# Kernel optimization log

Hardware: AMD Instinct MI355X
Metric: run time of the kernel (lower is better)

The kernel has to match this reference:

```python
import jax, jax.numpy as jnp
import numpy as np

EMBED = 512
NHEAD = 16
HDIM = EMBED // NHEAD
HIDDEN = 512  # Mlp hidden is hard-coded to 512
EPS_LN = 1e-6
EPS_ATT = 1e-6


def layernorm(x, gamma, beta):
    mu = jnp.mean(x, axis=-1, keepdims=True)
    var = jnp.mean(jnp.square(x - mu), axis=-1, keepdims=True)
    return (x - mu) * jax.lax.rsqrt(var + EPS_LN) * gamma + beta


def setup_inputs() -> dict:
    key = jax.random.key(0)
    ks = jax.random.split(key, 16)
    B, N, C = 8, 4096, EMBED
    s = 1.0 / np.sqrt(C)
    inp = {
        "x": jax.random.normal(ks[0], (B, N, C), dtype=jnp.float32),
        # projection weights stored as (in, out); torch Linear uses x @ W.T
        "Wq": jax.random.normal(ks[1], (C, C), dtype=jnp.float32) * s,
        "Wk": jax.random.normal(ks[2], (C, C), dtype=jnp.float32) * s,
        "Wv": jax.random.normal(ks[3], (C, C), dtype=jnp.float32) * s,
        "Wm": jax.random.normal(ks[4], (C, C), dtype=jnp.float32) * s,
        "W1": jax.random.normal(ks[5], (C, HIDDEN), dtype=jnp.float32) * s,
        "b1": jax.random.normal(ks[6], (HIDDEN,), dtype=jnp.float32) * 1e-6,
        "W2": jax.random.normal(ks[7], (HIDDEN, C), dtype=jnp.float32) * (1.0 / np.sqrt(HIDDEN)),
        "b2": jax.random.normal(ks[8], (C,), dtype=jnp.float32) * 1e-6,
        "g_att": jnp.ones((C,), dtype=jnp.float32),
        "b_att": jnp.zeros((C,), dtype=jnp.float32),
        "g_ffn": jnp.ones((C,), dtype=jnp.float32),
        "b_ffn": jnp.zeros((C,), dtype=jnp.float32),
    }
    return inp


def reference(x, Wq, Wk, Wv, Wm, W1, b1, W2, b2, g_att, b_att, g_ffn, b_ffn):
    B, N, C = x.shape
    # --- attention sub-block ---
    h = layernorm(x, g_att, b_att)
    q = (h @ Wq).reshape(B, N, NHEAD, HDIM)
    k = (h @ Wk).reshape(B, N, NHEAD, HDIM)
    v = (h @ Wv).reshape(B, N, NHEAD, HDIM)
    Q = jax.nn.elu(q) + 1.0  # feature map: elu(x)+1
    K = jax.nn.elu(k) + 1.0
    v = v / N
    KV = jnp.einsum('nshd,nshv->nhdv', K, v)
    Z = 1.0 / (jnp.einsum('nlhd,nhd->nlh', Q, K.sum(axis=1)) + EPS_ATT)
    msg = jnp.einsum('nlhd,nhdv->nlhv', Q, KV) * Z[..., None] * N
    msg = msg.reshape(B, N, C) @ Wm
    x = x + msg
    # --- feed-forward sub-block ---
    h2 = layernorm(x, g_ffn, b_ffn)
    f = jax.nn.gelu(h2 @ W1 + b1, approximate=False) @ W2 + b2
    return x + f
```

## Files before the change

### kernel.cpp

```cpp
#include <hip/hip_runtime.h>
#include <hip/hip_bf16.h>
#include <math.h>

typedef unsigned short u16;
typedef __attribute__((ext_vector_type(8))) __bf16 bf16x8;
typedef __attribute__((ext_vector_type(4))) float floatx4;

#define SEQ   4096
#define BATCH 8
#define ROWS  32768
#define C     512
#define NH    16
#define HD    32

__device__ inline u16 f2bf(float f) {
    union { float f; unsigned u; } v; v.f = f;
    unsigned r = (v.u + 0x7FFFu + ((v.u >> 16) & 1u)) >> 16;
    return (u16)r;
}
__device__ inline float bf2f(u16 h) {
    union { unsigned u; float f; } v; v.u = ((unsigned)h) << 16;
    return v.f;
}

__device__ inline void g2lds16(const u16* g, u16* l) {
    __builtin_amdgcn_global_load_lds((const __attribute__((address_space(1))) unsigned*)g,
                                     (__attribute__((address_space(3))) unsigned*)l, 16, 0, 0);
}

__global__ __launch_bounds__(256) void prep_weights(
    const float* __restrict__ Wq, const float* __restrict__ Wk,
    const float* __restrict__ Wv, const float* __restrict__ Wm,
    const float* __restrict__ W1, const float* __restrict__ W2,
    u16* __restrict__ Wqkvt, u16* __restrict__ Wmt,
    u16* __restrict__ W1t, u16* __restrict__ W2t)
{
    int blk = blockIdx.x;
    int mat = blk >> 6;
    int tile = blk & 63;
    int k0 = (tile >> 3) * 64, n0 = (tile & 7) * 64;
    const float* src; u16* dst;
    switch (mat) {
        case 0: src = Wq; dst = Wqkvt;              break;
        case 1: src = Wk; dst = Wqkvt + 512*512;    break;
        case 2: src = Wv; dst = Wqkvt + 2*512*512;  break;
        case 3: src = Wm; dst = Wmt;                break;
        case 4: src = W1; dst = W1t;                break;
        default: src = W2; dst = W2t;               break;
    }
    __shared__ float ts[64][65];
    int t = threadIdx.x;
    #pragma unroll
    for (int i = 0; i < 16; i++) {
        int e = i * 256 + t;
        int kr = e >> 6, nc = e & 63;
        ts[kr][nc] = src[(size_t)(k0 + kr) * 512 + n0 + nc];
    }
    __syncthreads();
    #pragma unroll
    for (int i = 0; i < 2; i++) {
        int e = i * 256 + t;
        int nr = e >> 3, kc0 = (e & 7) * 8;
        union { uint4 v; u16 u[8]; } o;
        #pragma unroll
        for (int q = 0; q < 8; q++) o.u[q] = f2bf(ts[kc0 + q][nr]);
        *(uint4*)(dst + (size_t)(n0 + nr) * 512 + k0 + kc0) = o.v;
    }
}

__global__ __launch_bounds__(256) void ln_kernel(
    const float* __restrict__ in, const float* __restrict__ g,
    const float* __restrict__ b, u16* __restrict__ out)
{
    int row  = blockIdx.x * 4 + (threadIdx.x >> 6);
    int lane = threadIdx.x & 63;
    const float* p = in + (size_t)row * C + lane * 8;
    float4 v0 = *(const float4*)p;
    float4 v1 = *(const float4*)(p + 4);
    float s  = v0.x + v0.y + v0.z + v0.w + v1.x + v1.y + v1.z + v1.w;
    float s2 = v0.x*v0.x + v0.y*v0.y + v0.z*v0.z + v0.w*v0.w
             + v1.x*v1.x + v1.y*v1.y + v1.z*v1.z + v1.w*v1.w;
    #pragma unroll
    for (int off = 1; off < 64; off <<= 1) {
        s  += __shfl_xor(s, off);
        s2 += __shfl_xor(s2, off);
    }
    float mean = s * (1.f / C);
    float var  = s2 * (1.f / C) - mean * mean;
    float inv  = rsqrtf(var + 1e-6f);
    int c = lane * 8;
    float4 g0 = *(const float4*)(g + c), g1 = *(const float4*)(g + c + 4);
    float4 b0 = *(const float4*)(b + c), b1 = *(const float4*)(b + c + 4);
    union { uint4 v; u16 u[8]; } o;
    o.u[0] = f2bf((v0.x - mean) * inv * g0.x + b0.x);
    o.u[1] = f2bf((v0.y - mean) * inv * g0.y + b0.y);
    o.u[2] = f2bf((v0.z - mean) * inv * g0.z + b0.z);
    o.u[3] = f2bf((v0.w - mean) * inv * g0.w + b0.w);
    o.u[4] = f2bf((v1.x - mean) * inv * g1.x + b1.x);
    o.u[5] = f2bf((v1.y - mean) * inv * g1.y + b1.y);
    o.u[6] = f2bf((v1.z - mean) * inv * g1.z + b1.z);
    o.u[7] = f2bf((v1.w - mean) * inv * g1.w + b1.w);
    *(uint4*)(out + (size_t)row * C + c) = o.v;
}

template <int EPI>
__global__ __launch_bounds__(256, 2) void gemm_tile(
    const u16* __restrict__ A, const u16* __restrict__ Bt,
    int K, int ldc, int nyt,
    u16* __restrict__ outb, float* __restrict__ outf,
    const float* __restrict__ bias, const float* __restrict__ resid)
{
    __shared__ u16 lsA[128 * 64];
    __shared__ u16 lsB[128 * 64];
    const int t = threadIdx.x;
    const int w = t >> 6, l = t & 63, lr = l & 15, quad = l >> 4;
    const int g = blockIdx.x;
    const int xcd = g & 7;
    const int q = g >> 3;
    const int per = nyt >> 3;
    const int ty = xcd * per + (q % per);
    const int tx = q / per;
    const int m0 = ty * 128, n0 = tx * 128;
    const int RW = (w >> 1) * 64, CW = (w & 1) * 64;

    floatx4 acc[4][4];
    #pragma unroll
    for (int i = 0; i < 4; i++)
        #pragma unroll
        for (int j = 0; j < 4; j++) { floatx4 z = {0.f, 0.f, 0.f, 0.f}; acc[i][j] = z; }

    const int srow = w * 32 + (l >> 3);
    const int scol = (((l & 7) - (l >> 3)) & 7) * 8;
    const u16* Ag = A  + (size_t)(m0 + srow) * K + scol;
    const u16* Bg = Bt + (size_t)(n0 + srow) * K + scol;
    u16* lAw = lsA + w * 2048;
    u16* lBw = lsB + w * 2048;

    for (int kk = 0; kk < K; kk += 64) {
        __syncthreads();
        #pragma unroll
        for (int c = 0; c < 4; c++) {
            g2lds16(Ag + (size_t)(c * 8) * K + kk, lAw + c * 512);
            g2lds16(Bg + (size_t)(c * 8) * K + kk, lBw + c * 512);
        }
        __syncthreads();
        #pragma unroll
        for (int ks = 0; ks < 2; ks++) {
            bf16x8 af[4], bfr[4];
            const int m = ((ks * 4 + quad + (lr & 7)) & 7) * 8;
            #pragma unroll
            for (int i = 0; i < 4; i++) {
                af[i]  = *(const bf16x8*)(lsA + (RW + i * 16 + lr) * 64 + m);
                bfr[i] = *(const bf16x8*)(lsB + (CW + i * 16 + lr) * 64 + m);
            }
            #pragma unroll
            for (int i = 0; i < 4; i++)
                #pragma unroll
                for (int j = 0; j < 4; j++)
                    acc[i][j] = __builtin_amdgcn_mfma_f32_16x16x32_bf16(af[i], bfr[j], acc[i][j], 0, 0, 0);
        }
    }

    #pragma unroll
    for (int i = 0; i < 4; i++) {
        #pragma unroll
        for (int j = 0; j < 4; j++) {
            #pragma unroll
            for (int r = 0; r < 4; r++) {
                int row = m0 + RW + i * 16 + quad * 4 + r;
                int col = n0 + CW + j * 16 + lr;
                float v = acc[i][j][r];
                size_t idx = (size_t)row * ldc + col;
                if constexpr (EPI == 0) {
                    if (col < 1024) v = v > 0.f ? v + 1.f : __expf(v);
                    else            v *= (1.0f / SEQ);
                    outb[idx] = f2bf(v);
                } else if constexpr (EPI == 1) {
                    outf[idx] = resid[idx] + v;
                } else if constexpr (EPI == 2) {
                    v += bias[col];
                    v = 0.5f * v * (1.f + erff(v * 0.70710678118f));
                    outb[idx] = f2bf(v);
                } else {
                    outf[idx] = outf[idx] + v + bias[col];
                }
            }
        }
    }
}

__global__ __launch_bounds__(256) void kv_reduce(
    const u16* __restrict__ qkv, float* __restrict__ Pkv, float* __restrict__ PKsum)
{
    const int bh = blockIdx.x;
    const int b = bh >> 4, h = bh & 15;
    const int chunk = blockIdx.y;
    const int t = threadIdx.x;
    const int w = t >> 6, l = t & 63, lr = l & 15, quad = l >> 4;
    __shared__ u16 lds[4 * 2 * 2048];

    const int sbase = chunk * 512 + w * 128;
    const u16* qbase = qkv + (size_t)b * SEQ * 1536 + 512 + h * HD;

    const int sl0 = l >> 2;
    const int sl1 = 16 + sl0;
    const int cl  = l & 3;
    const int cg0 = (cl + (sl0 >> 3)) & 3;
    const int cg1 = (cl + (sl1 >> 3)) & 3;
    const int gof0 = sl0 * 1536 + cg0 * 8;
    const int gof1 = sl1 * 1536 + cg1 * 8;

    u16* myl = lds + w * 4096;

    const int offA0 = quad * 256 + ((((lr >> 3) + 0) - quad) & 3) * 8 + (lr & 7);
    const int offA1 = quad * 256 + ((((lr >> 3) + 2) - quad) & 3) * 8 + (lr & 7);

    floatx4 a00 = {0,0,0,0}, a01 = {0,0,0,0}, a10 = {0,0,0,0}, a11 = {0,0,0,0};
    float ks0 = 0.f, ks1 = 0.f;

    {
        const u16* gK = qbase + (size_t)sbase * 1536;
        g2lds16(gK + gof0,       myl);
        g2lds16(gK + gof1,       myl + 512);
        g2lds16(gK + 512 + gof0, myl + 1024);
        g2lds16(gK + 512 + gof1, myl + 1536);
    }
    #pragma unroll
    for (int st = 0; st < 4; st++) {
        if (st < 3) {
            const u16* gK = qbase + (size_t)(sbase + (st + 1) * 32) * 1536;
            u16* nl = myl + ((st + 1) & 1) * 2048;
            g2lds16(gK + gof0,       nl);
            g2lds16(gK + gof1,       nl + 512);
            g2lds16(gK + 512 + gof0, nl + 1024);
            g2lds16(gK + 512 + gof1, nl + 1536);
        }
        __syncthreads();
        const u16* lK = myl + (st & 1) * 2048;
        const u16* lV = lK + 1024;
        union { bf16x8 v; u16 u[8]; } fa0, fa1, fb0, fb1;
        #pragma unroll
        for (int j = 0; j < 8; j++) {
            fa0.u[j] = lK[offA0 + j * 32];
            fa1.u[j] = lK[offA1 + j * 32];
            fb0.u[j] = lV[offA0 + j * 32];
            fb1.u[j] = lV[offA1 + j * 32];
        }
        #pragma unroll
        for (int j = 0; j < 8; j++) { ks0 += bf2f(fa0.u[j]); ks1 += bf2f(fa1.u[j]); }
        a00 = __builtin_amdgcn_mfma_f32_16x16x32_bf16(fa0.v, fb0.v, a00, 0, 0, 0);
        a01 = __builtin_amdgcn_mfma_f32_16x16x32_bf16(fa0.v, fb1.v, a01, 0, 0, 0);
        a10 = __builtin_amdgcn_mfma_f32_16x16x32_bf16(fa1.v, fb0.v, a10, 0, 0, 0);
        a11 = __builtin_amdgcn_mfma_f32_16x16x32_bf16(fa1.v, fb1.v, a11, 0, 0, 0);
    }

    const int p = bh * 32 + chunk * 4 + w;
    float* dst = Pkv + (size_t)p * 1024;
    floatx4 accs[2][2] = {{a00, a01}, {a10, a11}};
    #pragma unroll
    for (int i = 0; i < 2; i++)
        #pragma unroll
        for (int j = 0; j < 2; j++)
            #pragma unroll
            for (int r = 0; r < 4; r++)
                dst[(i * 16 + quad * 4 + r) * 32 + j * 16 + lr] = accs[i][j][r];

    float k0 = ks0 + __shfl_xor(ks0, 16); k0 += __shfl_xor(k0, 32);
    float k1 = ks1 + __shfl_xor(ks1, 16); k1 += __shfl_xor(k1, 32);
    if (quad == 0) {
        PKsum[p * 32 + lr]      = k0;
        PKsum[p * 32 + 16 + lr] = k1;
    }
}

__global__ __launch_bounds__(256) void kv_final(
    const float* __restrict__ Pkv, const float* __restrict__ PKsum,
    float* __restrict__ KV, float* __restrict__ Ksum)
{
    const int bh = blockIdx.x;
    const int t = threadIdx.x;
    float a0 = 0.f, a1 = 0.f, a2 = 0.f, a3 = 0.f;
    for (int p = 0; p < 32; p++) {
        const float* src = Pkv + ((size_t)bh * 32 + p) * 1024;
        a0 += src[t];
        a1 += src[t + 256];
        a2 += src[t + 512];
        a3 += src[t + 768];
    }
    float* dst = KV + (size_t)bh * 1024;
    dst[t] = a0; dst[t + 256] = a1; dst[t + 512] = a2; dst[t + 768] = a3;
    if (t < 32) {
        float s = 0.f;
        for (int p = 0; p < 32; p++) s += PKsum[(bh * 32 + p) * 32 + t];
        Ksum[bh * 32 + t] = s;
    }
}

__global__ __launch_bounds__(256) void msg_kernel(
    const u16* __restrict__ qkv, const float* __restrict__ KV,
    const float* __restrict__ Ksum, u16* __restrict__ msg)
{
    int blk = blockIdx.x;
    int b = blk >> 7;
    int r0 = (blk & 127) * 32;
    int t = threadIdx.x;
    int h = t >> 4;
    int vd = (t & 15) * 2;
    float kv0[32], kv1[32], ksr[32];
    const float* kvh = KV + ((size_t)b * 16 + h) * 1024;
    const float* ksh = Ksum + (b * 16 + h) * 32;
    #pragma unroll
    for (int d = 0; d < 32; d++) {
        kv0[d] = kvh[d * 32 + vd];
        kv1[d] = kvh[d * 32 + vd + 1];
        ksr[d] = ksh[d];
    }
    __shared__ u16 Qs[4 * 512];
    const int srr = t >> 6;
    const int scc = (t & 63) * 8;
    for (int rg = 0; rg < 32; rg += 4) {
        size_t row = (size_t)b * SEQ + r0 + rg;
        uint4 qv = *(const uint4*)(qkv + (row + srr) * 1536 + scc);
        __syncthreads();
        *(uint4*)(Qs + srr * 512 + scc) = qv;
        __syncthreads();
        #pragma unroll
        for (int r2 = 0; r2 < 4; r2++) {
            const u16* qp = Qs + r2 * 512 + h * HD;
            float q[32];
            #pragma unroll
            for (int i0 = 0; i0 < 32; i0 += 8) {
                union { uint4 v; u16 u[8]; } uu;
                uu.v = *(const uint4*)(qp + i0);
                #pragma unroll
                for (int jq = 0; jq < 8; jq++) q[i0 + jq] = bf2f(uu.u[jq]);
            }
            float zdot = 0.f, m0 = 0.f, m1 = 0.f;
            #pragma unroll
            for (int d = 0; d < 32; d++) {
                float qd = q[d];
                zdot += qd * ksr[d];
                m0   += qd * kv0[d];
                m1   += qd * kv1[d];
            }
            float z = (float)SEQ / (zdot + 1e-6f);
            unsigned pack = (unsigned)f2bf(m0 * z) | ((unsigned)f2bf(m1 * z) << 16);
            *(unsigned*)(msg + (row + r2) * C + h * HD + vd) = pack;
        }
    }
}

extern "C" void kernel_launch(void* const* d_in, const int* in_sizes, int n_in,
                              void* d_out, int out_size, void* d_ws, size_t ws_size,
                              hipStream_t stream) {
    const float* x     = (const float*)d_in[0];
    const float* Wq    = (const float*)d_in[1];
    const float* Wk    = (const float*)d_in[2];
    const float* Wv    = (const float*)d_in[3];
    const float* Wm    = (const float*)d_in[4];
    const float* W1    = (const float*)d_in[5];
    const float* b1    = (const float*)d_in[6];
    const float* W2    = (const float*)d_in[7];
    const float* b2    = (const float*)d_in[8];
    const float* g_att = (const float*)d_in[9];
    const float* b_att = (const float*)d_in[10];
    const float* g_ffn = (const float*)d_in[11];
    const float* b_ffn = (const float*)d_in[12];
    float* out = (float*)d_out;

    char* ws = (char*)d_ws;
    u16*   Wqkvt = (u16*)(ws);
    u16*   Wmt   = (u16*)(ws + 0x180000);
    u16*   W1t   = (u16*)(ws + 0x200000);
    u16*   W2t   = (u16*)(ws + 0x280000);
    float* KV    = (float*)(ws + 0x300000);
    float* Ksum  = (float*)(ws + 0x380000);
    u16*   hb    = (u16*)(ws + 0x400000);
    float* Pkv   = (float*)(ws + 0x400000);
    float* PKsum = (float*)(ws + 0x1400000);
    u16*   qkv   = (u16*)(ws + 0x2400000);
    u16*   h2    = qkv;
    u16*   f1    = (u16*)(ws + 0x4400000);

    prep_weights<<<6 * 64, 256, 0, stream>>>(Wq, Wk, Wv, Wm, W1, W2,
                                             Wqkvt, Wmt, W1t, W2t);
    ln_kernel<<<ROWS / 4, 256, 0, stream>>>(x, g_att, b_att, hb);
    gemm_tile<0><<<12 * 256, 256, 0, stream>>>(hb, Wqkvt, 512, 1536, 256,
                                               qkv, nullptr, nullptr, nullptr);
    kv_reduce<<<dim3(128, 8), 256, 0, stream>>>(qkv, Pkv, PKsum);
    kv_final<<<128, 256, 0, stream>>>(Pkv, PKsum, KV, Ksum);
    msg_kernel<<<1024, 256, 0, stream>>>(qkv, KV, Ksum, hb);
    gemm_tile<1><<<4 * 256, 256, 0, stream>>>(hb, Wmt, 512, 512, 256,
                                              nullptr, out, nullptr, x);
    ln_kernel<<<ROWS / 4, 256, 0, stream>>>(out, g_ffn, b_ffn, h2);
    gemm_tile<2><<<4 * 256, 256, 0, stream>>>(h2, W1t, 512, 512, 256,
                                              f1, nullptr, b1, nullptr);
    gemm_tile<3><<<4 * 256, 256, 0, stream>>>(f1, W2t, 512, 512, 256,
                                              nullptr, out, b2, nullptr);
}
```

Before: 405.2 us.

## Replace 128x128 GEMM with 256x256 double-buffered, phase-pipelined 8-wave kernel

Replaces the single-buffered 128x128 GEMM tile with a 256x256 tile computed by 512 threads. The LDS is double-buffered and the work is split into quadrant phases, so global-to-LDS loads for later k-steps overlap the MFMA work, using explicit waitcnt, barriers and setprio. The larger tile raises operand reuse and cuts the number of blocks, but it uses more LDS and registers and hard-codes K=512 and the grid mapping. With 256 blocks for the N=512 GEMMs there may be barely one wave of blocks across the CUs.

```diff
diff --git a/kernel.cpp b/kernel.cpp
--- a/kernel.cpp
+++ b/kernel.cpp
@@ -103,72 +103,125 @@
     *(uint4*)(out + (size_t)row * C + c) = o.v;
 }
 
+
+#define STGA(S, H, KC)                                                          \
+  do {                                                                          \
+    const u16* _g = Ab + (size_t)((H) * 128) * 512 + (KC);                      \
+    u16* _l = &lsA[S][(H) * 8192 + w * 1024];                                   \
+    g2lds16(_g, _l);                                                            \
+    g2lds16(_g + 8 * 512, _l + 512);                                            \
+  } while (0)
+
+#define STGB(S, H, KC)                                                          \
+  do {                                                                          \
+    const u16* _g = Bb + (size_t)((H) * 128) * 512 + (KC);                      \
+    u16* _l = &lsB[S][(H) * 8192 + w * 1024];                                   \
+    g2lds16(_g, _l);                                                            \
+    g2lds16(_g + 8 * 512, _l + 512);                                            \
+  } while (0)
+
+#define PH(S, MH, NH, STG, VM)                                                  \
+  do {                                                                          \
+    bf16x8 af0[4], af1[4], bv0[2], bv1[2];                                      \
+    const u16* As_ = &lsA[S][(MH) * 8192 + aoff];                               \
+    const u16* Bs_ = &lsB[S][(NH) * 8192 + boff];                               \
+    _Pragma("unroll") for (int ii = 0; ii < 4; ii++) {                          \
+      af0[ii] = *(const bf16x8*)(As_ + ii * 1024 + ck0);                        \
+      af1[ii] = *(const bf16x8*)(As_ + ii * 1024 + ck1);                        \
+    }                                                                           \
+    _Pragma("unroll") for (int jj = 0; jj < 2; jj++) {                          \
+      bv0[jj] = *(const bf16x8*)(Bs_ + jj * 1024 + ck0);                        \
+      bv1[jj] = *(const bf16x8*)(Bs_ + jj * 1024 + ck1);                        \
+    }                                                                           \
+    STG;                                                                        \
+    __builtin_amdgcn_sched_barrier(0);                                          \
+    if constexpr ((VM) == 4) asm volatile("s_waitcnt vmcnt(4)" ::: "memory");   \
+    else if constexpr ((VM) == 0) asm volatile("s_waitcnt vmcnt(0)" ::: "memory"); \
+    __builtin_amdgcn_s_barrier();                                               \
+    asm volatile("s_waitcnt lgkmcnt(0)" ::: "memory");                          \
+    __builtin_amdgcn_sched_barrier(0);                                          \
+    __builtin_amdgcn_s_setprio(1);                                              \
+    _Pragma("unroll") for (int ii = 0; ii < 4; ii++)                            \
+      _Pragma("unroll") for (int jj = 0; jj < 2; jj++) {                        \
+        acc[(MH)*4+ii][(NH)*2+jj] = __builtin_amdgcn_mfma_f32_16x16x32_bf16(    \
+            af0[ii], bv0[jj], acc[(MH)*4+ii][(NH)*2+jj], 0, 0, 0);              \
+        acc[(MH)*4+ii][(NH)*2+jj] = __builtin_amdgcn_mfma_f32_16x16x32_bf16(    \
+            af1[ii], bv1[jj], acc[(MH)*4+ii][(NH)*2+jj], 0, 0, 0);              \
+      }                                                                         \
+    __builtin_amdgcn_s_setprio(0);                                              \
+    __builtin_amdgcn_s_barrier();                                               \
+  } while (0)
+
 template <int EPI>
-__global__ __launch_bounds__(256, 2) void gemm_tile(
+__global__ __launch_bounds__(512, 2) void gemm256(
     const u16* __restrict__ A, const u16* __restrict__ Bt,
-    int K, int ldc, int nyt,
+    int ldc, int nx,
     u16* __restrict__ outb, float* __restrict__ outf,
     const float* __restrict__ bias, const float* __restrict__ resid)
 {
-    __shared__ u16 lsA[128 * 64];
-    __shared__ u16 lsB[128 * 64];
+    __shared__ u16 lsA[2][16384];
+    __shared__ u16 lsB[2][16384];
     const int t = threadIdx.x;
     const int w = t >> 6, l = t & 63, lr = l & 15, quad = l >> 4;
+    const int wr = w >> 2, wc = w & 3;
+
     const int g = blockIdx.x;
     const int xcd = g & 7;
     const int q = g >> 3;
-    const int per = nyt >> 3;
-    const int ty = xcd * per + (q % per);
-    const int tx = q / per;
-    const int m0 = ty * 128, n0 = tx * 128;
-    const int RW = (w >> 1) * 64, CW = (w & 1) * 64;
-
-    floatx4 acc[4][4];
-    #pragma unroll
-    for (int i = 0; i < 4; i++)
+    const int grp = q / (nx * 2), rem = q - grp * (nx * 2);
+    const int tx = rem >> 1;
+    const int ty = xcd * 16 + grp * 2 + (rem & 1);
+    const int m0 = ty * 256, n0 = tx * 256;
+
+    const int rh = w * 16 + (l >> 3);
+    const int swz = (((l & 7) - (l >> 3)) & 7) * 8;
+    const u16* Ab = A  + (size_t)(m0 + rh) * 512 + swz;
+    const u16* Bb = Bt + (size_t)(n0 + rh) * 512 + swz;
+
+    const int aoff = (wr * 64 + lr) * 64;
+    const int boff = (wc * 32 + lr) * 64;
+    const int ck0 = (((0 + quad + (lr & 7)) & 7) * 8);
+    const int ck1 = (((4 + quad + (lr & 7)) & 7) * 8);
+
+    floatx4 acc[8][4];
+    #pragma unroll
+    for (int i = 0; i < 8; i++)
         #pragma unroll
         for (int j = 0; j < 4; j++) { floatx4 z = {0.f, 0.f, 0.f, 0.f}; acc[i][j] = z; }
 
-    const int srow = w * 32 + (l >> 3);
-    const int scol = (((l & 7) - (l >> 3)) & 7) * 8;
-    const u16* Ag = A  + (size_t)(m0 + srow) * K + scol;
-    const u16* Bg = Bt + (size_t)(n0 + srow) * K + scol;
-    u16* lAw = lsA + w * 2048;
-    u16* lBw = lsB + w * 2048;
-
-    for (int kk = 0; kk < K; kk += 64) {
-        __syncthreads();
-        #pragma unroll
-        for (int c = 0; c < 4; c++) {
-            g2lds16(Ag + (size_t)(c * 8) * K + kk, lAw + c * 512);
-            g2lds16(Bg + (size_t)(c * 8) * K + kk, lBw + c * 512);
-        }
-        __syncthreads();
-        #pragma unroll
-        for (int ks = 0; ks < 2; ks++) {
-            bf16x8 af[4], bfr[4];
-            const int m = ((ks * 4 + quad + (lr & 7)) & 7) * 8;
-            #pragma unroll
-            for (int i = 0; i < 4; i++) {
-                af[i]  = *(const bf16x8*)(lsA + (RW + i * 16 + lr) * 64 + m);
-                bfr[i] = *(const bf16x8*)(lsB + (CW + i * 16 + lr) * 64 + m);
-            }
-            #pragma unroll
-            for (int i = 0; i < 4; i++)
-                #pragma unroll
-                for (int j = 0; j < 4; j++)
-                    acc[i][j] = __builtin_amdgcn_mfma_f32_16x16x32_bf16(af[i], bfr[j], acc[i][j], 0, 0, 0);
-        }
-    }
-
-    #pragma unroll
-    for (int i = 0; i < 4; i++) {
+    STGA(0, 0, 0); STGA(0, 1, 0); STGB(0, 0, 0); STGB(0, 1, 0);
+    STGA(1, 0, 64); STGB(1, 1, 64);
+    asm volatile("s_waitcnt vmcnt(4)" ::: "memory");
+    __builtin_amdgcn_s_barrier();
+
+    int kk = 0;
+    for (int it = 0; it < 3; ++it, kk += 128) {
+        PH(0, 0, 0, STGA(1, 1, kk + 64),  -1);
+        PH(0, 0, 1, STGB(1, 0, kk + 64),  -1);
+        PH(0, 1, 1, STGA(0, 0, kk + 128), -1);
+        PH(0, 1, 0, STGB(0, 1, kk + 128),  4);
+        PH(1, 0, 0, STGA(0, 1, kk + 128), -1);
+        PH(1, 0, 1, STGB(0, 0, kk + 128), -1);
+        PH(1, 1, 1, STGA(1, 0, kk + 192), -1);
+        PH(1, 1, 0, STGB(1, 1, kk + 192),  4);
+    }
+    PH(0, 0, 0, STGA(1, 1, kk + 64), -1);
+    PH(0, 0, 1, STGB(1, 0, kk + 64), -1);
+    PH(0, 1, 1, (void)0, -1);
+    PH(0, 1, 0, (void)0,  0);
+    PH(1, 0, 0, (void)0, -1);
+    PH(1, 0, 1, (void)0, -1);
+    PH(1, 1, 1, (void)0, -1);
+    PH(1, 1, 0, (void)0, -1);
+
+    #pragma unroll
+    for (int i = 0; i < 8; i++) {
         #pragma unroll
         for (int j = 0; j < 4; j++) {
             #pragma unroll
             for (int r = 0; r < 4; r++) {
-                int row = m0 + RW + i * 16 + quad * 4 + r;
-                int col = n0 + CW + j * 16 + lr;
+                int row = m0 + (i >> 2) * 128 + wr * 64 + (i & 3) * 16 + quad * 4 + r;
+                int col = n0 + (j >> 1) * 128 + wc * 32 + (j & 1) * 16 + lr;
                 float v = acc[i][j][r];
                 size_t idx = (size_t)row * ldc + col;
                 if constexpr (EPI == 0) {
@@ -385,16 +438,16 @@
     prep_weights<<<6 * 64, 256, 0, stream>>>(Wq, Wk, Wv, Wm, W1, W2,
                                              Wqkvt, Wmt, W1t, W2t);
     ln_kernel<<<ROWS / 4, 256, 0, stream>>>(x, g_att, b_att, hb);
-    gemm_tile<0><<<12 * 256, 256, 0, stream>>>(hb, Wqkvt, 512, 1536, 256,
-                                               qkv, nullptr, nullptr, nullptr);
+    gemm256<0><<<768, 512, 0, stream>>>(hb, Wqkvt, 1536, 6,
+                                        qkv, nullptr, nullptr, nullptr);
     kv_reduce<<<dim3(128, 8), 256, 0, stream>>>(qkv, Pkv, PKsum);
     kv_final<<<128, 256, 0, stream>>>(Pkv, PKsum, KV, Ksum);
     msg_kernel<<<1024, 256, 0, stream>>>(qkv, KV, Ksum, hb);
-    gemm_tile<1><<<4 * 256, 256, 0, stream>>>(hb, Wmt, 512, 512, 256,
-                                              nullptr, out, nullptr, x);
+    gemm256<1><<<256, 512, 0, stream>>>(hb, Wmt, 512, 2,
+                                        nullptr, out, nullptr, x);
     ln_kernel<<<ROWS / 4, 256, 0, stream>>>(out, g_ffn, b_ffn, h2);
-    gemm_tile<2><<<4 * 256, 256, 0, stream>>>(h2, W1t, 512, 512, 256,
-                                              f1, nullptr, b1, nullptr);
-    gemm_tile<3><<<4 * 256, 256, 0, stream>>>(f1, W2t, 512, 512, 256,
-                                              nullptr, out, b2, nullptr);
-}
+    gemm256<2><<<256, 512, 0, stream>>>(h2, W1t, 512, 2,
+                                        f1, nullptr, b1, nullptr);
+    gemm256<3><<<256, 512, 0, stream>>>(f1, W2t, 512, 2,
+                                        nullptr, out, b2, nullptr);
+}
```

New measurement: 595.5 us. 1.47x slower.

## Add LDS-resident B streaming GEMM for QKV projection and retile block mapping

Applied to the files above, without the earlier changes.

Adds a new 512-thread GEMM kernel for the QKV projection. It loads a full 64x512 slice of the transposed weight into LDS once and streams A in double-buffered 64-wide K chunks, with hand-scheduled ds_read_b128, MFMA 16x16x32 and setprio. The existing tile GEMM's block-to-tile mapping changes to group pairs of row tiles per XCD for cache locality. kv_final is split across four blocks per head to raise parallelism. The new kernel relies on inline asm and fixed waitcnt values, which ties correctness to exact instruction ordering.

```diff
diff --git a/kernel.cpp b/kernel.cpp
--- a/kernel.cpp
+++ b/kernel.cpp
@@ -27,6 +27,8 @@
     __builtin_amdgcn_global_load_lds((const __attribute__((address_space(1))) unsigned*)g,
                                      (__attribute__((address_space(3))) unsigned*)l, 16, 0, 0);
 }
+
+#define LDSA(p) ((unsigned)(size_t)(const __attribute__((address_space(3))) u16*)(p))
 
 __global__ __launch_bounds__(256) void prep_weights(
     const float* __restrict__ Wq, const float* __restrict__ Wk,
@@ -103,10 +105,152 @@
     *(uint4*)(out + (size_t)row * C + c) = o.v;
 }
 
+
+#define DSR(D, AR, OFFS) \
+    asm volatile("ds_read_b128 %0, %1 offset:" OFFS : "=v"(D) : "v"(AR))
+
+#define MFMA_(A, B, CC) __builtin_amdgcn_mfma_f32_16x16x32_bf16(                \
+    __builtin_bit_cast(bf16x8, A), __builtin_bit_cast(bf16x8, B), CC, 0, 0, 0)
+
+#define STGA_S(BUF, KK)                                                         \
+  do {                                                                          \
+    g2lds16(Ag + 0 * 4096 + (KK), Ald + (BUF) * 2048 + 0 * 512);                \
+    g2lds16(Ag + 1 * 4096 + (KK), Ald + (BUF) * 2048 + 1 * 512);                \
+    g2lds16(Ag + 2 * 4096 + (KK), Ald + (BUF) * 2048 + 2 * 512);                \
+    g2lds16(Ag + 3 * 4096 + (KK), Ald + (BUF) * 2048 + 3 * 512);                \
+  } while (0)
+
+#define GITER(VM, AO0, AO1, DODMA, BUF, KKN)                                    \
+  do {                                                                          \
+    asm volatile("s_waitcnt vmcnt(" VM ")");                                    \
+    __builtin_amdgcn_sched_barrier(0);                                          \
+    DSR(a00, vA0, AO0); DSR(a10, vA0, AO1);                                     \
+    DSR(a01, vA1, AO0); DSR(a11, vA1, AO1);                                     \
+    DSR(b00, vB0, "0");     DSR(b10, vB0, "16384");                             \
+    DSR(b20, vB0, "32768"); DSR(b30, vB0, "49152");                             \
+    DSR(b01, vB1, "0");     DSR(b11, vB1, "16384");                             \
+    DSR(b21, vB1, "32768"); DSR(b31, vB1, "49152");                             \
+    vB0 += 128; vB1 += 128;                                                     \
+    asm volatile("s_waitcnt lgkmcnt(0)");                                       \
+    __builtin_amdgcn_sched_barrier(0);                                          \
+    if (DODMA) { STGA_S(BUF, KKN); }                                            \
+    __builtin_amdgcn_sched_barrier(0);                                          \
+    __builtin_amdgcn_s_setprio(1);                                              \
+    acc[0][0] = MFMA_(a00, b00, acc[0][0]);                                     \
+    acc[0][1] = MFMA_(a00, b10, acc[0][1]);                                     \
+    acc[0][2] = MFMA_(a00, b20, acc[0][2]);                                     \
+    acc[0][3] = MFMA_(a00, b30, acc[0][3]);                                     \
+    acc[1][0] = MFMA_(a10, b00, acc[1][0]);                                     \
+    acc[1][1] = MFMA_(a10, b10, acc[1][1]);                                     \
+    acc[1][2] = MFMA_(a10, b20, acc[1][2]);                                     \
+    acc[1][3] = MFMA_(a10, b30, acc[1][3]);                                     \
+    acc[0][0] = MFMA_(a01, b01, acc[0][0]);                                     \
+    acc[0][1] = MFMA_(a01, b11, acc[0][1]);                                     \
+    acc[0][2] = MFMA_(a01, b21, acc[0][2]);                                     \
+    acc[0][3] = MFMA_(a01, b31, acc[0][3]);                                     \
+    acc[1][0] = MFMA_(a11, b01, acc[1][0]);                                     \
+    acc[1][1] = MFMA_(a11, b11, acc[1][1]);                                     \
+    acc[1][2] = MFMA_(a11, b21, acc[1][2]);                                     \
+    acc[1][3] = MFMA_(a11, b31, acc[1][3]);                                     \
+    __builtin_amdgcn_s_setprio(0);                                              \
+  } while (0)
+
+template <int EPI>
+__global__ __launch_bounds__(512, 2) void gemm_stream(
+    const u16* __restrict__ A, const u16* __restrict__ Bt,
+    int ldc, int nx,
+    u16* __restrict__ outb, float* __restrict__ outf,
+    const float* __restrict__ bias, const float* __restrict__ resid)
+{
+    __shared__ u16 LSD[65536];
+    const int t = threadIdx.x;
+    const int w = t >> 6, l = t & 63, lr = l & 15, quad = l >> 4;
+
+    const int g = blockIdx.x;
+    const int xcd = g & 7;
+    const int q = g >> 3;
+    const int npg = nx * 2;
+    const int grp = q / npg, rem = q - grp * npg;
+    const int tx = rem >> 1;
+    const int ty = xcd * 16 + grp * 2 + (rem & 1);
+    const int wm0 = ty * 256 + w * 32;
+    const int n0  = tx * 64;
+
+    const int brow = w * 8;
+    #pragma unroll
+    for (int j = 0; j < 8; j++) {
+        int r = brow + j;
+        const u16* src = Bt + (size_t)(n0 + r) * 512 + (((l & 56) | ((l - r) & 7)) * 8);
+        g2lds16(src, (u16*)&LSD[r * 512]);
+    }
+
+    const int arow = l >> 3;
+    const int aswz = (((l & 7) - arow) & 7) * 8;
+    const u16* Ag = A + (size_t)(wm0 + arow) * 512 + aswz;
+    u16* Ald = (u16*)&LSD[32768 + w * 4096];
+
+    STGA_S(0, 0);
+    STGA_S(1, 64);
+    __builtin_amdgcn_sched_barrier(0);
+    asm volatile("s_waitcnt vmcnt(8)");
+    __builtin_amdgcn_s_barrier();
+    __builtin_amdgcn_sched_barrier(0);
+
+    const int ck0 = ((0 + quad + (lr & 7)) & 7) * 8;
+    const int ck1 = ((4 + quad + (lr & 7)) & 7) * 8;
+    unsigned vB0 = LDSA(LSD + lr * 512 + ck0);
+    unsigned vB1 = LDSA(LSD + lr * 512 + ck1);
+    unsigned vA0 = LDSA(LSD + 32768 + w * 4096 + lr * 64 + ck0);
+    unsigned vA1 = LDSA(LSD + 32768 + w * 4096 + lr * 64 + ck1);
+
+    floatx4 acc[2][4];
+    #pragma unroll
+    for (int i = 0; i < 2; i++)
+        #pragma unroll
+        for (int j = 0; j < 4; j++) { floatx4 z = {0.f, 0.f, 0.f, 0.f}; acc[i][j] = z; }
+    floatx4 a00, a01, a10, a11, b00, b10, b20, b30, b01, b11, b21, b31;
+
+    GITER("4", "0",    "2048", 1, 0, 128);
+    GITER("4", "4096", "6144", 1, 1, 192);
+    GITER("4", "0",    "2048", 1, 0, 256);
+    GITER("4", "4096", "6144", 1, 1, 320);
+    GITER("4", "0",    "2048", 1, 0, 384);
+    GITER("4", "4096", "6144", 1, 1, 448);
+    GITER("4", "0",    "2048", 0, 0, 0);
+    GITER("0", "4096", "6144", 0, 1, 0);
+
+    #pragma unroll
+    for (int i = 0; i < 2; i++) {
+        #pragma unroll
+        for (int nf = 0; nf < 4; nf++) {
+            #pragma unroll
+            for (int r = 0; r < 4; r++) {
+                int row = wm0 + i * 16 + quad * 4 + r;
+                int col = n0 + nf * 16 + lr;
+                float v = acc[i][nf][r];
+                size_t idx = (size_t)row * ldc + col;
+                if constexpr (EPI == 0) {
+                    if (col < 1024) v = v > 0.f ? v + 1.f : __expf(v);
+                    else            v *= (1.0f / SEQ);
+                    outb[idx] = f2bf(v);
+                } else if constexpr (EPI == 1) {
+                    outf[idx] = resid[idx] + v;
+                } else if constexpr (EPI == 2) {
+                    v += bias[col];
+                    v = 0.5f * v * (1.f + erff(v * 0.70710678118f));
+                    outb[idx] = f2bf(v);
+                } else {
+                    outf[idx] = outf[idx] + v + bias[col];
+                }
+            }
+        }
+    }
+}
+
 template <int EPI>
 __global__ __launch_bounds__(256, 2) void gemm_tile(
     const u16* __restrict__ A, const u16* __restrict__ Bt,
-    int K, int ldc, int nyt,
+    int K, int ldc, int nx,
     u16* __restrict__ outb, float* __restrict__ outf,
     const float* __restrict__ bias, const float* __restrict__ resid)
 {
@@ -117,9 +261,10 @@
     const int g = blockIdx.x;
     const int xcd = g & 7;
     const int q = g >> 3;
-    const int per = nyt >> 3;
-    const int ty = xcd * per + (q % per);
-    const int tx = q / per;
+    const int npg = nx * 2;
+    const int grp = q / npg, rem = q - grp * npg;
+    const int tx = rem >> 1;
+    const int ty = xcd * 32 + grp * 2 + (rem & 1);
     const int m0 = ty * 128, n0 = tx * 128;
     const int RW = (w >> 1) * 64, CW = (w & 1) * 64;
 
@@ -277,19 +422,15 @@
     const float* __restrict__ Pkv, const float* __restrict__ PKsum,
     float* __restrict__ KV, float* __restrict__ Ksum)
 {
-    const int bh = blockIdx.x;
+    const int blk = blockIdx.x;
+    const int bh = blk >> 2, part = blk & 3;
     const int t = threadIdx.x;
-    float a0 = 0.f, a1 = 0.f, a2 = 0.f, a3 = 0.f;
-    for (int p = 0; p < 32; p++) {
-        const float* src = Pkv + ((size_t)bh * 32 + p) * 1024;
-        a0 += src[t];
-        a1 += src[t + 256];
-        a2 += src[t + 512];
-        a3 += src[t + 768];
-    }
-    float* dst = KV + (size_t)bh * 1024;
-    dst[t] = a0; dst[t + 256] = a1; dst[t + 512] = a2; dst[t + 768] = a3;
-    if (t < 32) {
+    const float* src = Pkv + (size_t)bh * 32 * 1024 + part * 256 + t;
+    float a = 0.f;
+    #pragma unroll 4
+    for (int p = 0; p < 32; p++) a += src[(size_t)p * 1024];
+    KV[(size_t)bh * 1024 + part * 256 + t] = a;
+    if (part == 0 && t < 32) {
         float s = 0.f;
         for (int p = 0; p < 32; p++) s += PKsum[(bh * 32 + p) * 32 + t];
         Ksum[bh * 32 + t] = s;
@@ -385,16 +526,16 @@
     prep_weights<<<6 * 64, 256, 0, stream>>>(Wq, Wk, Wv, Wm, W1, W2,
                                              Wqkvt, Wmt, W1t, W2t);
     ln_kernel<<<ROWS / 4, 256, 0, stream>>>(x, g_att, b_att, hb);
-    gemm_tile<0><<<12 * 256, 256, 0, stream>>>(hb, Wqkvt, 512, 1536, 256,
-                                               qkv, nullptr, nullptr, nullptr);
+    gemm_stream<0><<<3072, 512, 0, stream>>>(hb, Wqkvt, 1536, 24,
+                                             qkv, nullptr, nullptr, nullptr);
     kv_reduce<<<dim3(128, 8), 256, 0, stream>>>(qkv, Pkv, PKsum);
-    kv_final<<<128, 256, 0, stream>>>(Pkv, PKsum, KV, Ksum);
+    kv_final<<<512, 256, 0, stream>>>(Pkv, PKsum, KV, Ksum);
     msg_kernel<<<1024, 256, 0, stream>>>(qkv, KV, Ksum, hb);
-    gemm_tile<1><<<4 * 256, 256, 0, stream>>>(hb, Wmt, 512, 512, 256,
+    gemm_tile<1><<<4 * 256, 256, 0, stream>>>(hb, Wmt, 512, 512, 4,
                                               nullptr, out, nullptr, x);
     ln_kernel<<<ROWS / 4, 256, 0, stream>>>(out, g_ffn, b_ffn, h2);
-    gemm_tile<2><<<4 * 256, 256, 0, stream>>>(h2, W1t, 512, 512, 256,
+    gemm_tile<2><<<4 * 256, 256, 0, stream>>>(h2, W1t, 512, 512, 4,
                                               f1, nullptr, b1, nullptr);
-    gemm_tile<3><<<4 * 256, 256, 0, stream>>>(f1, W2t, 512, 512, 256,
+    gemm_tile<3><<<4 * 256, 256, 0, stream>>>(f1, W2t, 512, 512, 4,
                                               nullptr, out, b2, nullptr);
 }
```

Measured after the change: 392.4 us. -3.2%, faster.
